# Kernel optimization log

Hardware: AMD Instinct MI355X
Metric: run time of the kernel (lower is better)

Reference implementation:

```python
import jax, jax.numpy as jnp
import numpy as np

J = 24           # joints
CIN_PJ = 4       # channels_in per joint  (C_in = 96)
COUT_PJ = 8      # channels_out per joint (C_out = 192)
K = 15           # kernel size
PAD = 7          # reflect padding on both sides (stride 1 -> T_out == T)
B, T = 128, 4096

NEIGHBOURS = [sorted({max(0, i - 1), i, min(J - 1, i + 1)}) for i in range(J)]

def _build_mask():
    # Block-sparse skeleton neighbour mask over the conv weight.
    mask = np.zeros((J * COUT_PJ, J * CIN_PJ, K), np.float32)
    for i, nb in enumerate(NEIGHBOURS):
        cols = [k * CIN_PJ + c for k in nb for c in range(CIN_PJ)]
        mask[i * COUT_PJ:(i + 1) * COUT_PJ, cols, :] = 1.0
    return jnp.asarray(mask)

MASK = _build_mask()  # [C_out, C_in, K]

def setup_inputs() -> dict:
    key = jax.random.key(0)
    kx, kw, kb = jax.random.split(key, 3)
    x = jax.random.normal(kx, (B, J * CIN_PJ, T), dtype=jnp.float32)
    weight = jax.random.normal(kw, (J * COUT_PJ, J * CIN_PJ, K), dtype=jnp.float32) * 0.05
    bias = jax.random.normal(kb, (J * COUT_PJ,), dtype=jnp.float32) * 0.05
    return {"x": x, "weight": weight, "bias": bias}

def reference(x, weight, bias):
    # weight masked by fixed skeleton-neighbour sparsity every forward pass
    w = weight * MASK
    # reflect-pad the time axis, then VALID conv1d (matches F.pad + conv1d(padding=0))
    xp = jnp.pad(x, ((0, 0), (0, 0), (PAD, PAD)), mode='reflect')
    out = jax.lax.conv_general_dilated(
        xp, w,
        window_strides=(1,),
        padding='VALID',
        dimension_numbers=('NCH', 'OIH', 'NCH'))
    return out + bias[None, :, None]
```

## Files before the change

### kernel.cpp

```cpp
#include <hip/hip_runtime.h>
#include <stdint.h>

#define TLEN  4096
#define BATCH 128
#define NG    6
#define TT    256
#define ROWS  272

typedef short short8 __attribute__((ext_vector_type(8)));
typedef float f32x4 __attribute__((ext_vector_type(4)));
typedef unsigned int uint;

__device__ __forceinline__ unsigned short f2bf(float f) {
    unsigned int u = __float_as_uint(f);
    u += 0x7fffu + ((u >> 16) & 1u);
    return (unsigned short)(u >> 16);
}

__global__ __launch_bounds__(256) void prep_weights_kernel(
    const float* __restrict__ w, unsigned short* __restrict__ wf)
{
    int e = blockIdx.x * 256 + threadIdx.x;
    int kk   = e & 255;
    int co_l = (e >> 8) & 15;
    int p    = e >> 12;
    int k    = kk >> 4;
    int ci_l = kk & 15;
    int jo = 2 * p + (co_l >> 3);
    int jn = 2 * p - 1 + (ci_l >> 2);
    int ci_g = 8 * p - 4 + ci_l;
    float v = 0.0f;
    if (k < 15 && jn >= 0 && jn < 24 && jn >= jo - 1 && jn <= jo + 1)
        v = w[((size_t)(16 * p + co_l) * 96 + ci_g) * 15 + k];
    wf[e] = f2bf(v);
}

__global__ __launch_bounds__(256, 4) void skel_conv_kernel(
    const float* __restrict__ x, const unsigned short* __restrict__ wf,
    const float* __restrict__ bias, float* __restrict__ out)
{
    __shared__ __align__(16) unsigned short xlds[ROWS * 24];

    const int tid  = threadIdx.x;
    const int t0   = blockIdx.x * TT;
    const int g    = blockIdx.y;
    const int b    = blockIdx.z;
    const int lane = tid & 63;
    const int wave = tid >> 6;
    const int q     = wave & 1;
    const int thalf = wave >> 1;
    const int p     = 2 * g + q;
    const int col  = lane & 15;
    const int hi2  = lane >> 4;

    short8 afrag[8];
    {
        const unsigned short* wp = wf + (size_t)(p * 16 + col) * 256 + hi2 * 8;
        #pragma unroll
        for (int s = 0; s < 8; ++s)
            afrag[s] = *reinterpret_cast<const short8*>(wp + s * 32);
    }
    #pragma unroll
    for (int s = 0; s < 8; ++s)
        asm volatile("" : "+v"(afrag[s]));

    {
        const int ciBase = 16 * g - 4;
        const float* xb = x + (size_t)b * 96 * TLEN;
        for (int r = tid; r < ROWS; r += 256) {
            uint vals[12];
            if (r < 270) {
                int tg = t0 - 7 + r;
                int src = tg < 0 ? -tg : (tg >= TLEN ? 2 * TLEN - 2 - tg : tg);
                const float* xs = xb + src;
                #pragma unroll
                for (int qq = 0; qq < 12; ++qq) {
                    int c0 = ciBase + 2 * qq;
                    int c1 = c0 + 1;
                    float f0 = ((unsigned)c0 < 96u) ? xs[(size_t)c0 * TLEN] : 0.f;
                    float f1 = ((unsigned)c1 < 96u) ? xs[(size_t)c1 * TLEN] : 0.f;
                    vals[qq] = (uint)f2bf(f0) | ((uint)f2bf(f1) << 16);
                }
            } else {
                #pragma unroll
                for (int qq = 0; qq < 12; ++qq) vals[qq] = 0u;
            }
            *reinterpret_cast<uint4*>(&xlds[r * 24 + 0]) =
                make_uint4(vals[0], vals[1], vals[2], vals[3]);
            *reinterpret_cast<uint4*>(&xlds[r * 24 + 8]) =
                make_uint4(vals[4], vals[5], vals[6], vals[7]);
            *reinterpret_cast<uint4*>(&xlds[r * 24 + 16]) =
                make_uint4(vals[8], vals[9], vals[10], vals[11]);
        }
    }
    __syncthreads();

    const int ci0 = 8 * q + 8 * (hi2 & 1);
    const int kb  = hi2 >> 1;
    const int colb = 4 * hi2;

    f32x4 acc[8];
    {
        float bv0 = bias[16 * p + colb + 0];
        float bv1 = bias[16 * p + colb + 1];
        float bv2 = bias[16 * p + colb + 2];
        float bv3 = bias[16 * p + colb + 3];
        #pragma unroll
        for (int nf = 0; nf < 8; ++nf)
            acc[nf] = (f32x4){bv0, bv1, bv2, bv3};
    }

    const int rbase = thalf * 128 + col + kb;
    #pragma unroll
    for (int s = 0; s < 8; ++s) {
        const unsigned short* bp = &xlds[(rbase + 2 * s) * 24 + ci0];
        #pragma unroll
        for (int nf = 0; nf < 8; ++nf) {
            short8 bfrag = *reinterpret_cast<const short8*>(bp + nf * (16 * 24));
            acc[nf] = __builtin_amdgcn_mfma_f32_16x16x32_bf16(afrag[s], bfrag, acc[nf], 0, 0, 0);
        }
    }

    float* ob = out + ((size_t)b * 192 + 16 * p + colb) * TLEN
              + t0 + thalf * 128 + col;
    #pragma unroll
    for (int nf = 0; nf < 8; ++nf) {
        #pragma unroll
        for (int r = 0; r < 4; ++r)
            ob[(size_t)r * TLEN + nf * 16] = acc[nf][r];
    }
}

extern "C" void kernel_launch(void* const* d_in, const int* in_sizes, int n_in,
                              void* d_out, int out_size, void* d_ws, size_t ws_size,
                              hipStream_t stream) {
    const float* x    = (const float*)d_in[0];
    const float* w    = (const float*)d_in[1];
    const float* bias = (const float*)d_in[2];
    float* out        = (float*)d_out;
    unsigned short* wf = (unsigned short*)d_ws;

    prep_weights_kernel<<<dim3(192), dim3(256), 0, stream>>>(w, wf);
    skel_conv_kernel<<<dim3(TLEN / TT, NG, BATCH), dim3(256), 0, stream>>>(
        x, wf, bias, out);
}
```

Before: 162.6 us.

## Make conv blocks persistent over four time tiles with double-buffered LDS staging

Each block now processes four consecutive 256-step time tiles instead of one. The global loads for the next tile are issued into registers before the MFMA loop of the current tile, then written to an alternate LDS buffer afterwards. This is meant to hide global-load latency behind compute and to amortise the weight-fragment and bias loads across more work. In exchange the grid has a quarter as many blocks, LDS use doubles, and the staged values take 26 more registers, which may lower occupancy.

```diff
diff --git a/kernel.cpp b/kernel.cpp
--- a/kernel.cpp
+++ b/kernel.cpp
@@ -5,6 +5,7 @@
 #define BATCH 128
 #define NG    6
 #define TT    256
+#define NIT   4
 #define ROWS  272
 
 typedef short short8 __attribute__((ext_vector_type(8)));
@@ -12,9 +13,12 @@
 typedef unsigned int uint;
 
 __device__ __forceinline__ unsigned short f2bf(float f) {
-    unsigned int u = __float_as_uint(f);
+    uint u = __float_as_uint(f);
     u += 0x7fffu + ((u >> 16) & 1u);
     return (unsigned short)(u >> 16);
+}
+__device__ __forceinline__ int reflect(int tg) {
+    return tg < 0 ? -tg : (tg >= TLEN ? 2 * TLEN - 2 - tg : tg);
 }
 
 __global__ __launch_bounds__(256) void prep_weights_kernel(
@@ -39,10 +43,10 @@
     const float* __restrict__ x, const unsigned short* __restrict__ wf,
     const float* __restrict__ bias, float* __restrict__ out)
 {
-    __shared__ __align__(16) unsigned short xlds[ROWS * 24];
+    __shared__ __align__(16) unsigned short xlds[2][ROWS * 24];
 
     const int tid  = threadIdx.x;
-    const int t0   = blockIdx.x * TT;
+    const int tb0  = blockIdx.x * (TT * NIT);
     const int g    = blockIdx.y;
     const int b    = blockIdx.z;
     const int lane = tid & 63;
@@ -52,6 +56,9 @@
     const int p     = 2 * g + q;
     const int col  = lane & 15;
     const int hi2  = lane >> 4;
+
+    const int ciBase = 16 * g - 4;
+    const float* xb = x + (size_t)b * 96 * TLEN;
 
     short8 afrag[8];
     {
@@ -64,70 +71,84 @@
     for (int s = 0; s < 8; ++s)
         asm volatile("" : "+v"(afrag[s]));
 
-    {
-        const int ciBase = 16 * g - 4;
-        const float* xb = x + (size_t)b * 96 * TLEN;
-        for (int r = tid; r < ROWS; r += 256) {
-            uint vals[12];
-            if (r < 270) {
-                int tg = t0 - 7 + r;
-                int src = tg < 0 ? -tg : (tg >= TLEN ? 2 * TLEN - 2 - tg : tg);
-                const float* xs = xb + src;
-                #pragma unroll
-                for (int qq = 0; qq < 12; ++qq) {
-                    int c0 = ciBase + 2 * qq;
-                    int c1 = c0 + 1;
-                    float f0 = ((unsigned)c0 < 96u) ? xs[(size_t)c0 * TLEN] : 0.f;
-                    float f1 = ((unsigned)c1 < 96u) ? xs[(size_t)c1 * TLEN] : 0.f;
-                    vals[qq] = (uint)f2bf(f0) | ((uint)f2bf(f1) << 16);
-                }
-            } else {
-                #pragma unroll
-                for (int qq = 0; qq < 12; ++qq) vals[qq] = 0u;
-            }
-            *reinterpret_cast<uint4*>(&xlds[r * 24 + 0]) =
-                make_uint4(vals[0], vals[1], vals[2], vals[3]);
-            *reinterpret_cast<uint4*>(&xlds[r * 24 + 8]) =
-                make_uint4(vals[4], vals[5], vals[6], vals[7]);
-            *reinterpret_cast<uint4*>(&xlds[r * 24 + 16]) =
-                make_uint4(vals[8], vals[9], vals[10], vals[11]);
+    const int colb = 4 * hi2;
+    float bv[4];
+    #pragma unroll
+    for (int r = 0; r < 4; ++r) bv[r] = bias[16 * p + colb + r];
+
+    const int hr  = 256 + (tid & 15);
+    const int hc0 = tid >> 4;
+    const int hc1 = 16 + (tid >> 4);
+
+    float v[24], hv0, hv1;
+
+    auto STAGE_ISSUE = [&](int tt0) {
+        int src = reflect(tt0 - 7 + tid);
+        const float* xs = xb + src;
+        #pragma unroll
+        for (int c = 0; c < 24; ++c) {
+            int cg = ciBase + c;
+            v[c] = ((unsigned)cg < 96u) ? xs[(size_t)cg * TLEN] : 0.f;
         }
-    }
+        int hsrc = reflect(tt0 - 7 + hr);
+        int cg0 = ciBase + hc0;
+        hv0 = (hr < 270 && (unsigned)cg0 < 96u) ? xb[(size_t)cg0 * TLEN + hsrc] : 0.f;
+        int cg1 = ciBase + hc1;
+        hv1 = (tid < 128 && hr < 270 && (unsigned)cg1 < 96u) ? xb[(size_t)cg1 * TLEN + hsrc] : 0.f;
+    };
+
+    auto STAGE_WRITE = [&](unsigned short* buf) {
+        uint vals[12];
+        #pragma unroll
+        for (int qq = 0; qq < 12; ++qq)
+            vals[qq] = (uint)f2bf(v[2 * qq]) | ((uint)f2bf(v[2 * qq + 1]) << 16);
+        *reinterpret_cast<uint4*>(&buf[tid * 24 + 0])  = make_uint4(vals[0], vals[1], vals[2],  vals[3]);
+        *reinterpret_cast<uint4*>(&buf[tid * 24 + 8])  = make_uint4(vals[4], vals[5], vals[6],  vals[7]);
+        *reinterpret_cast<uint4*>(&buf[tid * 24 + 16]) = make_uint4(vals[8], vals[9], vals[10], vals[11]);
+        buf[hr * 24 + hc0] = f2bf(hv0);
+        if (tid < 128) buf[hr * 24 + hc1] = f2bf(hv1);
+    };
+
+    STAGE_ISSUE(tb0);
+    STAGE_WRITE(xlds[0]);
     __syncthreads();
 
-    const int ci0 = 8 * q + 8 * (hi2 & 1);
-    const int kb  = hi2 >> 1;
-    const int colb = 4 * hi2;
+    const int ci0   = 8 * q + 8 * (hi2 & 1);
+    const int kb    = hi2 >> 1;
+    const int rbase = thalf * 128 + col + kb;
 
-    f32x4 acc[8];
-    {
-        float bv0 = bias[16 * p + colb + 0];
-        float bv1 = bias[16 * p + colb + 1];
-        float bv2 = bias[16 * p + colb + 2];
-        float bv3 = bias[16 * p + colb + 3];
+    #pragma unroll
+    for (int it = 0; it < NIT; ++it) {
+        const unsigned short* buf = xlds[it & 1];
+
+        if (it + 1 < NIT) STAGE_ISSUE(tb0 + (it + 1) * TT);
+
+        f32x4 acc[8];
         #pragma unroll
         for (int nf = 0; nf < 8; ++nf)
-            acc[nf] = (f32x4){bv0, bv1, bv2, bv3};
-    }
+            acc[nf] = (f32x4){bv[0], bv[1], bv[2], bv[3]};
 
-    const int rbase = thalf * 128 + col + kb;
-    #pragma unroll
-    for (int s = 0; s < 8; ++s) {
-        const unsigned short* bp = &xlds[(rbase + 2 * s) * 24 + ci0];
+        #pragma unroll
+        for (int s = 0; s < 8; ++s) {
+            const unsigned short* bp = &buf[(rbase + 2 * s) * 24 + ci0];
+            #pragma unroll
+            for (int nf = 0; nf < 8; ++nf) {
+                short8 bfrag = *reinterpret_cast<const short8*>(bp + nf * (16 * 24));
+                acc[nf] = __builtin_amdgcn_mfma_f32_16x16x32_bf16(afrag[s], bfrag, acc[nf], 0, 0, 0);
+            }
+        }
+
+        if (it + 1 < NIT) STAGE_WRITE(xlds[(it + 1) & 1]);
+        __syncthreads();
+
+        float* ob = out + ((size_t)b * 192 + 16 * p + colb) * TLEN
+                  + tb0 + it * TT + thalf * 128 + col;
         #pragma unroll
         for (int nf = 0; nf < 8; ++nf) {
-            short8 bfrag = *reinterpret_cast<const short8*>(bp + nf * (16 * 24));
-            acc[nf] = __builtin_amdgcn_mfma_f32_16x16x32_bf16(afrag[s], bfrag, acc[nf], 0, 0, 0);
+            #pragma unroll
+            for (int r = 0; r < 4; ++r)
+                ob[(size_t)r * TLEN + nf * 16] = acc[nf][r];
         }
-    }
-
-    float* ob = out + ((size_t)b * 192 + 16 * p + colb) * TLEN
-              + t0 + thalf * 128 + col;
-    #pragma unroll
-    for (int nf = 0; nf < 8; ++nf) {
-        #pragma unroll
-        for (int r = 0; r < 4; ++r)
-            ob[(size_t)r * TLEN + nf * 16] = acc[nf][r];
     }
 }
 
@@ -141,6 +162,6 @@
     unsigned short* wf = (unsigned short*)d_ws;
 
     prep_weights_kernel<<<dim3(192), dim3(256), 0, stream>>>(w, wf);
-    skel_conv_kernel<<<dim3(TLEN / TT, NG, BATCH), dim3(256), 0, stream>>>(
+    skel_conv_kernel<<<dim3(TLEN / (TT * NIT), NG, BATCH), dim3(256), 0, stream>>>(
         x, wf, bias, out);
 }
```

After: 162.7 us. About the same (+0.1%).
